# Performance work log

Hardware: AMD Instinct MI355X
Metric: run time of the kernel (lower is better)

The kernel has to match this reference:

```python
import jax, jax.numpy as jnp
import numpy as np

KERNEL = 5
PAD = (KERNEL - 1) // 2  # fixed_padding with dilation=1: pad_beg = pad_end = 2


def setup_inputs() -> dict:
    key = jax.random.key(0)
    kx, kw = jax.random.split(key)
    x = jax.random.normal(kx, (4, 4, 1024, 1024), dtype=jnp.float32)
    weight = jax.random.normal(kw, (4, 4, KERNEL, KERNEL), dtype=jnp.float32)
    return {"x": x, "weight": weight}


def reference(x, weight):
    """Morphological dilation2d: out[b,o,h,w] = max_{c,i,j} (x_pad[b,c,h+i,w+j] + w[o,c,i,j]).

    Equivalent to the torch unfold + broadcast-add + max over dim C*k*k, but computed
    as a fused sliding-window max-plus without materializing the im2col tensor.
    """
    B, C, H, W = x.shape
    k = weight.shape[-1]
    xp = jnp.pad(x, ((0, 0), (0, 0), (PAD, PAD), (PAD, PAD)))  # zero pad, same as F.pad
    out = None
    for i in range(k):
        for j in range(k):
            patch = xp[:, :, i:i + H, j:j + W]          # (B, C, H, W)
            w_ij = weight[:, :, i, j]                    # (O, C)
            # max over in_channels of (x + w) for this tap
            val = jnp.max(patch[:, None] + w_ij[None, :, :, None, None], axis=2)  # (B, O, H, W)
            out = val if out is None else jnp.maximum(out, val)
    return out
```

## Files before the change

### kernel.cpp

```cpp
#include <hip/hip_runtime.h>


constexpr int Himg = 1024, Wimg = 1024, Cin = 4, Cout = 4, Kn = 5;
constexpr int TH = 8, TW = 128;
constexpr int LR = TH + 4;
constexpr int LC = TW + 8;
constexpr int LC4 = LC / 4;
constexpr int NW = Cout * Cin * Kn * Kn;

typedef float v2f __attribute__((ext_vector_type(2)));

__device__ __align__(16) v2f wdup[Cin * Kn * Cout * Kn];

__global__ void reorg_w(const float* __restrict__ w) {
  int idx = threadIdx.x;
  if (idx < NW) {
    int o  = idx / (Cin * Kn * Kn);
    int r  = idx % (Cin * Kn * Kn);
    int c  = r / (Kn * Kn);
    int r2 = r % (Kn * Kn);
    int i  = r2 / Kn, j = r2 % Kn;
    float v = w[idx];
    v2f p; p.x = v; p.y = v;
    wdup[((c * Kn + i) * Cout + o) * Kn + j] = p;
  }
}

__device__ __forceinline__ float max5(float a, float b, float c, float d, float e) {
  return fmaxf(fmaxf(a, b), fmaxf(c, fmaxf(d, e)));
}

__global__ __launch_bounds__(256, 4) void morph(const float* __restrict__ x,
                                                float* __restrict__ out) {
  __shared__ __align__(16) float xs[Cin][LR][LC];
  const int tid = threadIdx.x;
  const int tile_w0 = blockIdx.x * TW;
  const int tile_r0 = blockIdx.y * TH;
  const int b = blockIdx.z;

  for (int idx = tid; idx < Cin * LR * LC4; idx += 256) {
    const int c   = idx / (LR * LC4);
    const int rem = idx - c * (LR * LC4);
    const int row = rem / LC4;
    const int ch  = rem - row * LC4;
    const int gr  = tile_r0 - 2 + row;
    const int gc  = tile_w0 - 4 + ch * 4;
    float4 v = make_float4(0.f, 0.f, 0.f, 0.f);
    if ((unsigned)gr < (unsigned)Himg) {
      const float* src = x + ((size_t)(b * Cin + c) * Himg + gr) * Wimg;
      if (gc >= 0 && gc <= Wimg - 4) {
        v = *(const float4*)(src + gc);
      } else {
        if ((unsigned)(gc + 0) < (unsigned)Wimg) v.x = src[gc + 0];
        if ((unsigned)(gc + 1) < (unsigned)Wimg) v.y = src[gc + 1];
        if ((unsigned)(gc + 2) < (unsigned)Wimg) v.z = src[gc + 2];
        if ((unsigned)(gc + 3) < (unsigned)Wimg) v.w = src[gc + 3];
      }
    }
    *(float4*)&xs[c][row][ch * 4] = v;
  }
  __syncthreads();

  const int tx = tid & 31;
  const int ty = tid >> 5;

  float acc[Cout][4];
#pragma unroll
  for (int o = 0; o < Cout; ++o)
#pragma unroll
    for (int p = 0; p < 4; ++p) acc[o][p] = -3.4e38f;

#define ACC_O(O, WDP)                                                                     \
  do {                                                                                    \
    v2f p01[5], p23[5];                                                                   \
    _Pragma("unroll") for (int j = 0; j < 5; ++j) {                                       \
      v2f wb = (WDP)[(O) * Kn + j];                                                       \
      p01[j] = a2[j] + wb;                                                                \
      p23[j] = b2[j] + wb;                                                                \
    }                                                                                     \
    acc[O][0] = fmaxf(acc[O][0], max5(p01[0].x, p01[1].x, p01[2].x, p01[3].x, p01[4].x)); \
    acc[O][1] = fmaxf(acc[O][1], max5(p01[0].y, p01[1].y, p01[2].y, p01[3].y, p01[4].y)); \
    acc[O][2] = fmaxf(acc[O][2], max5(p23[0].x, p23[1].x, p23[2].x, p23[3].x, p23[4].x)); \
    acc[O][3] = fmaxf(acc[O][3], max5(p23[0].y, p23[1].y, p23[2].y, p23[3].y, p23[4].y)); \
  } while (0)

#pragma unroll 1
  for (int c = 0; c < Cin; ++c) {
    float4 qa[Kn][3];
#pragma unroll
    for (int dr = 0; dr < Kn; ++dr) {
      const float* rowp = &xs[c][ty + dr][tx * 4];
      qa[dr][0] = *(const float4*)(rowp);
      qa[dr][1] = *(const float4*)(rowp + 4);
      qa[dr][2] = *(const float4*)(rowp + 8);
    }

#pragma unroll
    for (int i = 0; i < Kn; ++i) {
      const float win[12] = {qa[i][0].x, qa[i][0].y, qa[i][0].z, qa[i][0].w,
                             qa[i][1].x, qa[i][1].y, qa[i][1].z, qa[i][1].w,
                             qa[i][2].x, qa[i][2].y, qa[i][2].z, qa[i][2].w};

      v2f a2[5], b2[5];
#pragma unroll
      for (int j = 0; j < 5; ++j) {
        a2[j].x = win[2 + j]; a2[j].y = win[3 + j];
        b2[j].x = win[4 + j]; b2[j].y = win[5 + j];
      }

      const v2f* wdp = wdup + (c * Kn + i) * Cout * Kn;

      ACC_O(0, wdp);
      ACC_O(1, wdp);
      ACC_O(2, wdp);
      ACC_O(3, wdp);
    }
  }
#undef ACC_O

  const int r = tile_r0 + ty;
  const int gc0 = tile_w0 + tx * 4;
#pragma unroll
  for (int o = 0; o < Cout; ++o) {
    float4 res = make_float4(acc[o][0], acc[o][1], acc[o][2], acc[o][3]);
    *(float4*)&out[((size_t)(b * Cout + o) * Himg + r) * Wimg + gc0] = res;
  }
}

extern "C" void kernel_launch(void* const* d_in, const int* in_sizes, int n_in,
                              void* d_out, int out_size, void* d_ws, size_t ws_size,
                              hipStream_t stream) {
  const float* x = (const float*)d_in[0];
  const float* w = (const float*)d_in[1];
  float* out = (float*)d_out;

  reorg_w<<<dim3(1), dim3(512), 0, stream>>>(w);

  dim3 grid(Wimg / TW, Himg / TH, 4);
  morph<<<grid, dim3(256), 0, stream>>>(x, out);
}
```

Before: 153.3 us.

## Replace shared-memory tile staging with direct global loads per thread

Removes the LDS halo tile, its cooperative load loop, and the block barrier. Each thread instead reads its 12-wide window rows straight from global memory, relying on L1/L2 caching for the overlap between neighbouring threads and rows. The launch_bounds occupancy hint is also dropped. The trade is more redundant global/L1 traffic and latency exposed inside the compute loop, in exchange for no LDS use and no synchronisation.

```diff
diff --git a/kernel.cpp b/kernel.cpp
--- a/kernel.cpp
+++ b/kernel.cpp
@@ -3,9 +3,6 @@
 
 constexpr int Himg = 1024, Wimg = 1024, Cin = 4, Cout = 4, Kn = 5;
 constexpr int TH = 8, TW = 128;
-constexpr int LR = TH + 4;
-constexpr int LC = TW + 8;
-constexpr int LC4 = LC / 4;
 constexpr int NW = Cout * Cin * Kn * Kn;
 
 typedef float v2f __attribute__((ext_vector_type(2)));
@@ -30,39 +27,18 @@
   return fmaxf(fmaxf(a, b), fmaxf(c, fmaxf(d, e)));
 }
 
-__global__ __launch_bounds__(256, 4) void morph(const float* __restrict__ x,
-                                                float* __restrict__ out) {
-  __shared__ __align__(16) float xs[Cin][LR][LC];
+__global__ __launch_bounds__(256) void morph(const float* __restrict__ x,
+                                             float* __restrict__ out) {
   const int tid = threadIdx.x;
   const int tile_w0 = blockIdx.x * TW;
   const int tile_r0 = blockIdx.y * TH;
   const int b = blockIdx.z;
 
-  for (int idx = tid; idx < Cin * LR * LC4; idx += 256) {
-    const int c   = idx / (LR * LC4);
-    const int rem = idx - c * (LR * LC4);
-    const int row = rem / LC4;
-    const int ch  = rem - row * LC4;
-    const int gr  = tile_r0 - 2 + row;
-    const int gc  = tile_w0 - 4 + ch * 4;
-    float4 v = make_float4(0.f, 0.f, 0.f, 0.f);
-    if ((unsigned)gr < (unsigned)Himg) {
-      const float* src = x + ((size_t)(b * Cin + c) * Himg + gr) * Wimg;
-      if (gc >= 0 && gc <= Wimg - 4) {
-        v = *(const float4*)(src + gc);
-      } else {
-        if ((unsigned)(gc + 0) < (unsigned)Wimg) v.x = src[gc + 0];
-        if ((unsigned)(gc + 1) < (unsigned)Wimg) v.y = src[gc + 1];
-        if ((unsigned)(gc + 2) < (unsigned)Wimg) v.z = src[gc + 2];
-        if ((unsigned)(gc + 3) < (unsigned)Wimg) v.w = src[gc + 3];
-      }
-    }
-    *(float4*)&xs[c][row][ch * 4] = v;
-  }
-  __syncthreads();
-
   const int tx = tid & 31;
   const int ty = tid >> 5;
+
+  const int gb = tile_w0 + tx * 4 - 4;
+  const bool colsafe = (gb >= 0) && (gb + 12 <= Wimg);
 
   float acc[Cout][4];
 #pragma unroll
@@ -86,20 +62,31 @@
 
 #pragma unroll 1
   for (int c = 0; c < Cin; ++c) {
-    float4 qa[Kn][3];
-#pragma unroll
-    for (int dr = 0; dr < Kn; ++dr) {
-      const float* rowp = &xs[c][ty + dr][tx * 4];
-      qa[dr][0] = *(const float4*)(rowp);
-      qa[dr][1] = *(const float4*)(rowp + 4);
-      qa[dr][2] = *(const float4*)(rowp + 8);
-    }
-
+    const float* __restrict__ plane = x + (size_t)(b * Cin + c) * Himg * Wimg;
 #pragma unroll
     for (int i = 0; i < Kn; ++i) {
-      const float win[12] = {qa[i][0].x, qa[i][0].y, qa[i][0].z, qa[i][0].w,
-                             qa[i][1].x, qa[i][1].y, qa[i][1].z, qa[i][1].w,
-                             qa[i][2].x, qa[i][2].y, qa[i][2].z, qa[i][2].w};
+      const int gr = tile_r0 + ty + i - 2;
+      float win[12];
+#pragma unroll
+      for (int e = 0; e < 12; ++e) win[e] = 0.f;
+
+      if ((unsigned)gr < (unsigned)Himg) {
+        const float* srcr = plane + (size_t)gr * Wimg;
+        if (colsafe) {
+          float4 q0 = *(const float4*)(srcr + gb);
+          float4 q1 = *(const float4*)(srcr + gb + 4);
+          float4 q2 = *(const float4*)(srcr + gb + 8);
+          win[0] = q0.x; win[1]  = q0.y; win[2]  = q0.z; win[3]  = q0.w;
+          win[4] = q1.x; win[5]  = q1.y; win[6]  = q1.z; win[7]  = q1.w;
+          win[8] = q2.x; win[9]  = q2.y; win[10] = q2.z; win[11] = q2.w;
+        } else {
+#pragma unroll
+          for (int e = 0; e < 12; ++e) {
+            const int col = gb + e;
+            if ((unsigned)col < (unsigned)Wimg) win[e] = srcr[col];
+          }
+        }
+      }
 
       v2f a2[5], b2[5];
 #pragma unroll
```

Measured after the change: 218.9 us. +42.8%, slower.
